# Performance work log

Measured on AMD Instinct MI355X. Metric: run time of the kernel, lower is better.

## Reference

```python
import jax, jax.numpy as jnp
import numpy as np

HEADS = 16
DIM_HEAD = 64


def shift(x):
    # Transformer-XL relative shift trick. x: [..., i, j] -> [..., i, j]
    *lead, i, j = x.shape
    x = jnp.concatenate([x, jnp.zeros((*lead, i, i), x.dtype)], axis=-1)
    l = i + j - 1
    x = x.reshape(*lead, -1)
    pad = (-x.shape[-1]) % l
    x = jnp.concatenate([x, jnp.zeros((*lead, pad), x.dtype)], axis=-1)
    x = x.reshape(*lead, -1, l)
    return x[..., :i, i - 1:]


def setup_inputs() -> dict:
    key = jax.random.key(0)
    ks = jax.random.split(key, 6)
    b, t, d = 4, 1024, 1024
    mem_len = 1024
    s = 0.02
    return {
        "x": jax.random.normal(ks[0], (b, t, d), jnp.float32),
        "mem": jax.random.normal(ks[1], (b, mem_len, d), jnp.float32),
        "wq": jax.random.normal(ks[2], (d, d), jnp.float32) * s,
        "wkv": jax.random.normal(ks[3], (d, 2 * d), jnp.float32) * s,
        "wo": jax.random.normal(ks[4], (d, d), jnp.float32) * s,
        "bo": jnp.zeros((d,), jnp.float32),
        "rel_w": jax.random.normal(ks[5], (t + mem_len, HEADS, DIM_HEAD), jnp.float32) * s,
    }


def reference(x, mem, wq, wkv, wo, bo, rel_w):
    b, t, d = x.shape
    h, dh = HEADS, DIM_HEAD
    mem_len = mem.shape[1]
    scale = dh ** -0.5

    q = x @ wq                                  # [b,t,d]
    kv_in = jnp.concatenate([mem, x], axis=1)   # [b,t+mem,d]
    k, v = jnp.split(kv_in @ wkv, 2, axis=-1)

    to_heads = lambda z: z.reshape(b, -1, h, dh).transpose(0, 2, 1, 3)
    q, k, v = to_heads(q), to_heads(k), to_heads(v)  # [b,h,*,dh]

    dots = jnp.einsum('bhid,bhjd->bhij', q, k) * scale      # [b,h,t,t+mem]
    w = rel_w[: t + mem_len]                                 # [t+mem,h,dh]
    pos = shift(jnp.einsum('bhid,jhd->bhij', q, w) * scale)  # [b,h,t,t+mem]
    dots = dots + pos

    jdim = t + mem_len
    mask = jnp.triu(jnp.ones((t, jdim), bool), k=1 + mem_len)
    dots = jnp.where(mask[None, None], -jnp.inf, dots)
    attn = jax.nn.softmax(dots, axis=-1)

    out = jnp.einsum('bhij,bhjd->bhid', attn, v)
    out = out.transpose(0, 2, 1, 3).reshape(b, t, d)
    out = out @ wo + bo

    mem_next = jnp.concatenate([mem, x], axis=1)[:, -mem_len:]  # t == seq_len branch
    return out, mem_next
```

## Files before the change

### kernel.cpp

```cpp
#include <hip/hip_runtime.h>
#include <cstddef>
#include <cstdint>

#define B_DIM 4
#define T_DIM 1024
#define D_DIM 1024
#define H_DIM 16
#define DH 64
#define JDIM 2048
#define MEMLEN 1024
#define RELPAD 2176

typedef float floatx4 __attribute__((ext_vector_type(4)));
typedef short short8 __attribute__((ext_vector_type(8)));

static __device__ __forceinline__ short f2bf(float f) {
    union { float f; uint32_t u; } v; v.f = f;
    uint32_t r = (v.u + 0x7FFFu + ((v.u >> 16) & 1u)) >> 16;
    return (short)r;
}

static __device__ __forceinline__ void gl_lds16(const short* g, short* l) {
    __builtin_amdgcn_global_load_lds(
        (const __attribute__((address_space(1))) void*)g,
        (__attribute__((address_space(3))) void*)l, 16, 0, 0);
}

template <int CTRL>
static __device__ __forceinline__ float dpp_fmax(float v) {
    int y = __builtin_amdgcn_update_dpp(0, __builtin_bit_cast(int, v),
                                        CTRL, 0xF, 0xF, true);
    return fmaxf(v, __builtin_bit_cast(float, y));
}
static __device__ __forceinline__ float row16_max(float v) {
    v = dpp_fmax<0xB1>(v);
    v = dpp_fmax<0x4E>(v);
    v = dpp_fmax<0x124>(v);
    v = dpp_fmax<0x128>(v);
    return v;
}

__global__ __launch_bounds__(256) void prep_xmem(const float* __restrict__ x,
                                                 const float* __restrict__ mem,
                                                 float* __restrict__ mem_next,
                                                 short* __restrict__ kvb) {
    const size_t gid = (size_t)blockIdx.x * 256 + threadIdx.x;
    if (gid < 1048576) {
        const size_t idx = gid * 4;
        float4 v = *(const float4*)(x + idx);
        *(float4*)(mem_next + idx) = v;
        const int b = (int)(idx >> 20);
        const size_t r = idx & 1048575;
        short4 o;
        o.x = f2bf(v.x); o.y = f2bf(v.y); o.z = f2bf(v.z); o.w = f2bf(v.w);
        *(short4*)(kvb + (size_t)b * 2097152 + 1048576 + r) = o;
    } else {
        const size_t idx = (gid - 1048576) * 4;
        float4 v = *(const float4*)(mem + idx);
        const int b = (int)(idx >> 20);
        const size_t r = idx & 1048575;
        short4 o;
        o.x = f2bf(v.x); o.y = f2bf(v.y); o.z = f2bf(v.z); o.w = f2bf(v.w);
        *(short4*)(kvb + (size_t)b * 2097152 + r) = o;
    }
}

__global__ __launch_bounds__(256) void transpose_w3(
    const float* __restrict__ wq, const float* __restrict__ wkv,
    const float* __restrict__ wo, short* __restrict__ wkvqT,
    short* __restrict__ woT) {
    const int z = blockIdx.z;
    const int N = (z == 1) ? 2048 : 1024;
    if (blockIdx.y * 32 >= N) return;
    const float* w = (z == 0) ? wq : (z == 1) ? wkv : wo;
    short* wT = (z == 0) ? (wkvqT + (size_t)2048 * 1024) : (z == 1) ? wkvqT : woT;
    __shared__ float tile[32][33];
    const int k0 = blockIdx.x * 32, n0 = blockIdx.y * 32;
    const int tx = threadIdx.x, ty = threadIdx.y;
    for (int r = ty; r < 32; r += 8)
        tile[r][tx] = w[(size_t)(k0 + r) * N + n0 + tx];
    __syncthreads();
    for (int r = ty; r < 32; r += 8)
        wT[(size_t)(n0 + r) * 1024 + k0 + tx] = f2bf(tile[tx][r]);
}

__global__ __launch_bounds__(256) void convert_rel(const float* __restrict__ rel,
                                                   short* __restrict__ relb) {
    const int h = blockIdx.y;
    const int jp = blockIdx.x * 16 + (threadIdx.x >> 4);
    const int c = (threadIdx.x & 15) << 2;
    float4 v = make_float4(0.f, 0.f, 0.f, 0.f);
    if (jp < JDIM) v = *(const float4*)(rel + ((size_t)jp * H_DIM + h) * DH + c);
    short4 o;
    o.x = f2bf(v.x); o.y = f2bf(v.y); o.z = f2bf(v.z); o.w = f2bf(v.w);
    *(short4*)(relb + ((size_t)h * RELPAD + jp) * DH + c) = o;
}

template <int CMODE>
__global__ __launch_bounds__(256) void mfma_gemm(
    const short* __restrict__ A, const short* __restrict__ Bt,
    const float* __restrict__ bias,
    short* __restrict__ C0, short* __restrict__ C1, short* __restrict__ C2,
    float* __restrict__ Cf) {
    constexpr int K = 1024;
    const int row0 = blockIdx.y << 7, col0 = blockIdx.x << 7;
    if (CMODE == 1 && col0 >= 2048 && (row0 & 2047) < 1024) return;

    __shared__ short ash[128 * 32];
    __shared__ short bsh[128 * 32];

    const int tid = threadIdx.x;
    const int w = tid >> 6, lane = tid & 63;
    const int l15 = lane & 15, quad = lane >> 4;
    const int wr = w >> 1, wc = w & 1;

    const int sk = (lane & 3) << 3;
    const short* ap0 = A + (size_t)(row0 + (w << 5) + (lane >> 2)) * K + sk;
    const short* ap1 = ap0 + (size_t)16 * K;
    const short* bp0 = Bt + (size_t)(col0 + (w << 5) + (lane >> 2)) * K + sk;
    const short* bp1 = bp0 + (size_t)16 * K;

    floatx4 acc[4][4] = {};

    for (int k0 = 0; k0 < K; k0 += 32) {
        __syncthreads();
        gl_lds16(ap0 + k0, ash + (w << 10));
        gl_lds16(ap1 + k0, ash + (w << 10) + 512);
        gl_lds16(bp0 + k0, bsh + (w << 10));
        gl_lds16(bp1 + k0, bsh + (w << 10) + 512);
        __syncthreads();

        short8 af[4];
#pragma unroll
        for (int mt = 0; mt < 4; ++mt)
            af[mt] = *(const short8*)&ash[(((wr << 6) + (mt << 4) + l15) << 5) + (quad << 3)];
#pragma unroll
        for (int nt = 0; nt < 4; ++nt) {
            short8 bf = *(const short8*)&bsh[(((wc << 6) + (nt << 4) + l15) << 5) + (quad << 3)];
#pragma unroll
            for (int mt = 0; mt < 4; ++mt)
                acc[mt][nt] = __builtin_amdgcn_mfma_f32_16x16x32_bf16(af[mt], bf, acc[mt][nt], 0, 0, 0);
        }
    }

#pragma unroll
    for (int nt = 0; nt < 4; ++nt) {
        const int col = col0 + (wc << 6) + (nt << 4) + l15;
        float bv = (CMODE == 2) ? bias[col] : 0.f;
#pragma unroll
        for (int mt = 0; mt < 4; ++mt) {
#pragma unroll
            for (int rr = 0; rr < 4; ++rr) {
                const int row = row0 + (wr << 6) + (mt << 4) + (quad << 2) + rr;
                const float val = acc[mt][nt][rr];
                if (CMODE == 1) {
                    int b = row >> 11, j = row & 2047;
                    if (col < 1024) {
                        int h = col >> 6, c = col & 63;
                        C0[(((size_t)b * H_DIM + h) * JDIM + j) * DH + c] = f2bf(val);
                    } else if (col < 2048) {
                        int n2 = col - 1024, h = n2 >> 6, c = n2 & 63;
                        C1[(((size_t)b * H_DIM + h) * DH + c) * JDIM + j] = f2bf(val);
                    } else {
                        int n2 = col - 2048, h = n2 >> 6, c = n2 & 63;
                        int i = j - 1024;
                        C2[(((size_t)b * H_DIM + h) * T_DIM + i) * DH + c] =
                            f2bf(val * 0.18033688f);
                    }
                } else {
                    Cf[(size_t)row * 1024 + col] = val + bv;
                }
            }
        }
    }
}

__global__ __launch_bounds__(256, 4) void flash_attn(
    const short* __restrict__ qb, const short* __restrict__ kb,
    const short* __restrict__ vTb, const short* __restrict__ relb,
    short* __restrict__ ob) {
    __shared__ short kshf[8 * 512];
    __shared__ short vshf[8 * 512];
    __shared__ short rshf[3 * 8 * 512];

    const int tid = threadIdx.x;
    const int w = tid >> 6;
    const int lane = tid & 63;
    const int l15 = lane & 15, quad = lane >> 4;
    const int bh = blockIdx.y, h = bh & 15, b = bh >> 4;
    const int xt = blockIdx.x;
    const int itile = ((xt >> 2) + ((xt & 3) << 2) + (((blockIdx.y >> 4) & 3) << 2)) & 15;
    const int i0 = itile << 6;
    const int goff = 3 - w;

    const short* kb_b = kb + (size_t)bh * JDIM * DH;
    const short* vT_b = vTb + (size_t)bh * DH * JDIM;
    const short* rel_b = relb + (size_t)h * RELPAD * DH;

    const short* qrow = qb + ((size_t)bh * T_DIM + i0 + (w << 4) + l15) * DH;
    const short8 a_q0 = *(const short8*)(qrow + (quad << 3));
    const short8 a_q1 = *(const short8*)(qrow + 32 + (quad << 3));

    const int kc0 = w, kc1 = w + 4;
    const short* kp0 = kb_b + (size_t)(((kc0 >> 1) << 4) + l15) * DH + (kc0 & 1) * 32 + (quad << 3);
    const short* kp1 = kb_b + (size_t)(((kc1 >> 1) << 4) + l15) * DH + (kc1 & 1) * 32 + (quad << 3);
    const short* vp0 = vT_b + (size_t)(((kc0 >> 1) << 4) + l15) * JDIM + (kc0 & 1) * 32 + (quad << 3);
    const short* vp1 = vT_b + (size_t)(((kc1 >> 1) << 4) + l15) * JDIM + (kc1 & 1) * 32 + (quad << 3);
    const int base00 = 960 - i0;

    gl_lds16(kp0, kshf + (kc0 << 9));
    gl_lds16(kp1, kshf + (kc1 << 9));
    gl_lds16(vp0, vshf + (kc0 << 9));
    gl_lds16(vp1, vshf + (kc1 << 9));
    kp0 += 64 * DH; kp1 += 64 * DH; vp0 += 64; vp1 += 64;
#pragma unroll
    for (int s = 0; s < 4; ++s) {
        const int c4 = w + (s << 2);
        const short* rp = rel_b + (size_t)(base00 + ((c4 >> 1) << 4) + l15) * DH +
                          (c4 & 1) * 32 + (quad << 3);
        gl_lds16(rp, rshf + (c4 << 9));
    }
    const short* rw0 = rel_b + (size_t)(base00 + 128 + ((w >> 1) << 4) + l15) * DH +
                       (w & 1) * 32 + (quad << 3);
    const short* rw1 = rel_b + (size_t)(base00 + 128 + (((w + 4) >> 1) << 4) + l15) * DH +
                       ((w + 4) & 1) * 32 + (quad << 3);
    __syncthreads();

    short8 ones8;
#pragma unroll
    for (int z = 0; z < 8; ++z) ones8[z] = (short)0x3F80;

    int srcl[4], gsel[4];
#pragma unroll
    for (int r = 0; r < 4; ++r) {
        const int t = l15 - (quad << 2) - r + 15;
        gsel[r] = t >> 4;
        srcl[r] = (quad << 4) | (t & 15);
    }

    floatx4 o_acc[4] = {};
    float m_r[4], l_r[4];
#pragma unroll
    for (int r = 0; r < 4; ++r) { m_r[r] = -3.0e38f; l_r[r] = 0.f; }

    const int jt_end = itile + 17;
    int s0 = 0, s1 = 1, s2 = 2;

    for (int jt = 0; jt < jt_end; ++jt) {
        floatx4 s_acc[4];
#pragma unroll
        for (int nt = 0; nt < 4; ++nt) {
            short8 bk0 = *(const short8*)&kshf[((nt << 1) << 9) + (lane << 3)];
            short8 bk1 = *(const short8*)&kshf[(((nt << 1) + 1) << 9) + (lane << 3)];
            floatx4 acc = {0.f, 0.f, 0.f, 0.f};
            acc = __builtin_amdgcn_mfma_f32_16x16x32_bf16(a_q0, bk0, acc, 0, 0, 0);
            acc = __builtin_amdgcn_mfma_f32_16x16x32_bf16(a_q1, bk1, acc, 0, 0, 0);
            s_acc[nt] = acc;
        }

        floatx4 G[5];
#pragma unroll
        for (int gi = 0; gi < 5; ++gi) {
            const int rb = gi + goff;
            const int seg = (rb & 4) ? s1 : s0;
            const int ch = (seg << 3) + ((rb & 3) << 1);
            short8 br0 = *(const short8*)&rshf[(ch << 9) + (lane << 3)];
            short8 br1 = *(const short8*)&rshf[((ch + 1) << 9) + (lane << 3)];
            floatx4 acc = {0.f, 0.f, 0.f, 0.f};
            acc = __builtin_amdgcn_mfma_f32_16x16x32_bf16(a_q0, br0, acc, 0, 0, 0);
            G[gi] = __builtin_amdgcn_mfma_f32_16x16x32_bf16(a_q1, br1, acc, 0, 0, 0);
        }

        uint32_t pk[4][4];
#pragma unroll
        for (int gi = 0; gi < 4; ++gi)
#pragma unroll
            for (int r = 0; r < 4; ++r) {
                uint32_t g0 = __builtin_bit_cast(uint32_t, G[gi][r]);
                uint32_t g1 = __builtin_bit_cast(uint32_t, G[gi + 1][r]);
                pk[gi][r] = (g0 & 0xFFFF0000u) | (g1 >> 16);
            }
#pragma unroll
        for (int nt = 0; nt < 4; ++nt)
#pragma unroll
            for (int r = 0; r < 4; ++r) {
                uint32_t pv = (uint32_t)__shfl((int)pk[nt][r], srcl[r], 64);
                uint32_t gb = gsel[r] ? (pv << 16) : (pv & 0xFFFF0000u);
                s_acc[nt][r] = s_acc[nt][r] + __builtin_bit_cast(float, gb);
            }
        if (jt == jt_end - 1) {
#pragma unroll
            for (int nt = 0; nt < 4; ++nt) {
                const int u = (nt << 4) + l15;
#pragma unroll
                for (int r = 0; r < 4; ++r) {
                    const int v = (w << 4) + (quad << 2) + r;
                    if (u > v) s_acc[nt][r] = -3.0e38f;
                }
            }
        }

        __syncthreads();
        if (jt + 1 < jt_end) {
            gl_lds16(kp0, kshf + (kc0 << 9));
            gl_lds16(kp1, kshf + (kc1 << 9));
            gl_lds16(rw0, rshf + (s2 << 12) + (w << 9));
            gl_lds16(rw1, rshf + (s2 << 12) + ((w + 4) << 9));
            kp0 += 64 * DH; kp1 += 64 * DH; rw0 += 64 * DH; rw1 += 64 * DH;
        }

        short* pshp = rshf + (s0 << 12);

        float tm[4];
        bool need = false;
#pragma unroll
        for (int r = 0; r < 4; ++r) {
            tm[r] = fmaxf(fmaxf(s_acc[0][r], s_acc[1][r]),
                          fmaxf(s_acc[2][r], s_acc[3][r]));
            need |= (tm[r] > m_r[r] + 8.0f);
        }
        if (__any((int)need)) {
#pragma unroll
            for (int r = 0; r < 4; ++r) {
                const float t = row16_max(tm[r]);
                const float mx = fmaxf(m_r[r], t);
                const float alpha = __builtin_amdgcn_exp2f(m_r[r] - mx);
                m_r[r] = mx;
                l_r[r] *= alpha;
#pragma unroll
                for (int ct = 0; ct < 4; ++ct) o_acc[ct][r] *= alpha;
            }
        }
#pragma unroll
        for (int r = 0; r < 4; ++r) {
            const int prow = (w << 4) + (quad << 2) + r;
            char* rowb = (char*)pshp + (prow << 7);
            const int swz = (prow & 7) << 4;
#pragma unroll
            for (int nt = 0; nt < 4; ++nt) {
                const float p = __builtin_amdgcn_exp2f(s_acc[nt][r] - m_r[r]);
                *(short*)(rowb + ((((nt << 5) + (l15 << 1))) ^ swz)) = f2bf(p);
            }
        }

        const int arow = (w << 4) + l15;
        const char* arowb = (const char*)pshp + (arow << 7);
        const int asw = (l15 & 7) << 4;
        const short8 a_p0 = *(const short8*)(arowb + ((quad << 4) ^ asw));
        const short8 a_p1 = *(const short8*)(arowb + ((64 + (quad << 4)) ^ asw));
        floatx4 ls = {0.f, 0.f, 0.f, 0.f};
        ls = __builtin_amdgcn_mfma_f32_16x16x32_bf16(a_p0, ones8, ls, 0, 0, 0);
        ls = __builtin_amdgcn_mfma_f32_16x16x32_bf16(a_p1, ones8, ls, 0, 0, 0);
#pragma unroll
        for (int r = 0; r < 4; ++r) l_r[r] += ls[r];
#pragma unroll
        for (int ct = 0; ct < 4; ++ct) {
            short8 bv0 = *(const short8*)&vshf[((ct << 1) << 9) + (lane << 3)];
            short8 bv1 = *(const short8*)&vshf[(((ct << 1) + 1) << 9) + (lane << 3)];
            o_acc[ct] = __builtin_amdgcn_mfma_f32_16x16x32_bf16(a_p0, bv0, o_acc[ct], 0, 0, 0);
            o_acc[ct] = __builtin_amdgcn_mfma_f32_16x16x32_bf16(a_p1, bv1, o_acc[ct], 0, 0, 0);
        }

        __syncthreads();
        if (jt + 1 < jt_end) {
            gl_lds16(vp0, vshf + (kc0 << 9));
            gl_lds16(vp1, vshf + (kc1 << 9));
            vp0 += 64; vp1 += 64;
        }
        const int t = s0; s0 = s1; s1 = s2; s2 = t;
    }

#pragma unroll
    for (int ct = 0; ct < 4; ++ct) {
#pragma unroll
        for (int r = 0; r < 4; ++r) {
            const int i = i0 + (w << 4) + (quad << 2) + r;
            const float val = o_acc[ct][r] / l_r[r];
            ob[((size_t)b * T_DIM + i) * D_DIM + h * DH + (ct << 4) + l15] = f2bf(val);
        }
    }
}

extern "C" void kernel_launch(void* const* d_in, const int* in_sizes, int n_in,
                              void* d_out, int out_size, void* d_ws, size_t ws_size,
                              hipStream_t stream) {
    const float* x = (const float*)d_in[0];
    const float* mem = (const float*)d_in[1];
    const float* wq = (const float*)d_in[2];
    const float* wkv = (const float*)d_in[3];
    const float* wo = (const float*)d_in[4];
    const float* bo = (const float*)d_in[5];
    const float* rel_w = (const float*)d_in[6];

    float* out = (float*)d_out;
    float* mem_next = out + (size_t)B_DIM * T_DIM * D_DIM;

    short* kvb = (short*)d_ws;
    short* qb = kvb + 8388608;
    short* kb = qb + 4194304;
    short* vTb = kb + 8388608;
    short* relb = vTb + 8388608;
    short* ob = relb + 2228224;
    short* wkvqT = ob + 4194304;
    short* woT = wkvqT + 3145728;

    hipLaunchKernelGGL(prep_xmem, dim3(8192), dim3(256), 0, stream,
                       x, mem, mem_next, kvb);

    hipLaunchKernelGGL(transpose_w3, dim3(32, 64, 3), dim3(32, 8), 0, stream,
                       wq, wkv, wo, wkvqT, woT);

    hipLaunchKernelGGL(convert_rel, dim3(RELPAD / 16, H_DIM), dim3(256), 0, stream,
                       rel_w, relb);

    hipLaunchKernelGGL((mfma_gemm<1>), dim3(24, 64), dim3(256), 0, stream,
                       kvb, wkvqT, nullptr, kb, vTb, qb, nullptr);

    hipLaunchKernelGGL(flash_attn, dim3(16, 64), dim3(256), 0, stream,
                       qb, kb, vTb, relb, ob);

    hipLaunchKernelGGL((mfma_gemm<2>), dim3(8, 32), dim3(256), 0, stream,
                       ob, woT, bo, nullptr, nullptr, nullptr, out);
}
```

Measured before the change: 312.9 us.

## Merge prep kernels into one launch, add setprio and byte-perm packing

Folds the three preprocessing kernels (x/mem conversion, weight transposes, rel-embedding conversion) into a single kernel dispatched by block index, so two launches and their gaps go away. In flash attention, MFMA sections are wrapped in s_setprio to favour waves issuing matrix work. The bf16 packing and select logic is replaced with v_perm byte permutes. The early return inside the merged kernel's transpose branch happens before a __syncthreads, but it is uniform per block so it stays safe.

```diff
diff --git a/kernel.cpp b/kernel.cpp
--- a/kernel.cpp
+++ b/kernel.cpp
@@ -40,60 +40,65 @@
     return v;
 }
 
-__global__ __launch_bounds__(256) void prep_xmem(const float* __restrict__ x,
-                                                 const float* __restrict__ mem,
-                                                 float* __restrict__ mem_next,
-                                                 short* __restrict__ kvb) {
-    const size_t gid = (size_t)blockIdx.x * 256 + threadIdx.x;
-    if (gid < 1048576) {
-        const size_t idx = gid * 4;
-        float4 v = *(const float4*)(x + idx);
-        *(float4*)(mem_next + idx) = v;
-        const int b = (int)(idx >> 20);
-        const size_t r = idx & 1048575;
+__global__ __launch_bounds__(256) void prep_all(
+    const float* __restrict__ x, const float* __restrict__ mem,
+    const float* __restrict__ rel,
+    float* __restrict__ mem_next, short* __restrict__ kvb,
+    const float* __restrict__ wq, const float* __restrict__ wkv,
+    const float* __restrict__ wo, short* __restrict__ wkvqT,
+    short* __restrict__ woT, short* __restrict__ relb) {
+    __shared__ float tile[32][33];
+    const int bx = blockIdx.x;
+    const int tid = threadIdx.x;
+
+    if (bx < 8192) {
+        const size_t gid = (size_t)bx * 256 + tid;
+        if (gid < 1048576) {
+            const size_t idx = gid * 4;
+            float4 v = *(const float4*)(x + idx);
+            *(float4*)(mem_next + idx) = v;
+            const int b = (int)(idx >> 20);
+            const size_t r = idx & 1048575;
+            short4 o;
+            o.x = f2bf(v.x); o.y = f2bf(v.y); o.z = f2bf(v.z); o.w = f2bf(v.w);
+            *(short4*)(kvb + (size_t)b * 2097152 + 1048576 + r) = o;
+        } else {
+            const size_t idx = (gid - 1048576) * 4;
+            float4 v = *(const float4*)(mem + idx);
+            const int b = (int)(idx >> 20);
+            const size_t r = idx & 1048575;
+            short4 o;
+            o.x = f2bf(v.x); o.y = f2bf(v.y); o.z = f2bf(v.z); o.w = f2bf(v.w);
+            *(short4*)(kvb + (size_t)b * 2097152 + r) = o;
+        }
+    } else if (bx < 14336) {
+        const int i = bx - 8192;
+        const int z = i >> 11;
+        const int rem = i & 2047;
+        const int gx = rem & 31, gy = rem >> 5;
+        const int N = (z == 1) ? 2048 : 1024;
+        if (gy * 32 >= N) return;
+        const float* w = (z == 0) ? wq : (z == 1) ? wkv : wo;
+        short* wT = (z == 0) ? (wkvqT + (size_t)2048 * 1024) : (z == 1) ? wkvqT : woT;
+        const int k0 = gx * 32, n0 = gy * 32;
+        const int tx = tid & 31, ty = tid >> 5;
+        for (int r = ty; r < 32; r += 8)
+            tile[r][tx] = w[(size_t)(k0 + r) * N + n0 + tx];
+        __syncthreads();
+        for (int r = ty; r < 32; r += 8)
+            wT[(size_t)(n0 + r) * 1024 + k0 + tx] = f2bf(tile[tx][r]);
+    } else {
+        const int i = bx - 14336;
+        const int gx = i % 136, gy = i / 136;
+        const int h = gy;
+        const int jp = gx * 16 + (tid >> 4);
+        const int c = (tid & 15) << 2;
+        float4 v = make_float4(0.f, 0.f, 0.f, 0.f);
+        if (jp < JDIM) v = *(const float4*)(rel + ((size_t)jp * H_DIM + h) * DH + c);
         short4 o;
         o.x = f2bf(v.x); o.y = f2bf(v.y); o.z = f2bf(v.z); o.w = f2bf(v.w);
-        *(short4*)(kvb + (size_t)b * 2097152 + 1048576 + r) = o;
-    } else {
-        const size_t idx = (gid - 1048576) * 4;
-        float4 v = *(const float4*)(mem + idx);
-        const int b = (int)(idx >> 20);
-        const size_t r = idx & 1048575;
-        short4 o;
-        o.x = f2bf(v.x); o.y = f2bf(v.y); o.z = f2bf(v.z); o.w = f2bf(v.w);
-        *(short4*)(kvb + (size_t)b * 2097152 + r) = o;
-    }
-}
-
-__global__ __launch_bounds__(256) void transpose_w3(
-    const float* __restrict__ wq, const float* __restrict__ wkv,
-    const float* __restrict__ wo, short* __restrict__ wkvqT,
-    short* __restrict__ woT) {
-    const int z = blockIdx.z;
-    const int N = (z == 1) ? 2048 : 1024;
-    if (blockIdx.y * 32 >= N) return;
-    const float* w = (z == 0) ? wq : (z == 1) ? wkv : wo;
-    short* wT = (z == 0) ? (wkvqT + (size_t)2048 * 1024) : (z == 1) ? wkvqT : woT;
-    __shared__ float tile[32][33];
-    const int k0 = blockIdx.x * 32, n0 = blockIdx.y * 32;
-    const int tx = threadIdx.x, ty = threadIdx.y;
-    for (int r = ty; r < 32; r += 8)
-        tile[r][tx] = w[(size_t)(k0 + r) * N + n0 + tx];
-    __syncthreads();
-    for (int r = ty; r < 32; r += 8)
-        wT[(size_t)(n0 + r) * 1024 + k0 + tx] = f2bf(tile[tx][r]);
-}
-
-__global__ __launch_bounds__(256) void convert_rel(const float* __restrict__ rel,
-                                                   short* __restrict__ relb) {
-    const int h = blockIdx.y;
-    const int jp = blockIdx.x * 16 + (threadIdx.x >> 4);
-    const int c = (threadIdx.x & 15) << 2;
-    float4 v = make_float4(0.f, 0.f, 0.f, 0.f);
-    if (jp < JDIM) v = *(const float4*)(rel + ((size_t)jp * H_DIM + h) * DH + c);
-    short4 o;
-    o.x = f2bf(v.x); o.y = f2bf(v.y); o.z = f2bf(v.z); o.w = f2bf(v.w);
-    *(short4*)(relb + ((size_t)h * RELPAD + jp) * DH + c) = o;
+        *(short4*)(relb + ((size_t)h * RELPAD + jp) * DH + c) = o;
+    }
 }
 
 template <int CMODE>
@@ -230,11 +235,12 @@
 #pragma unroll
     for (int z = 0; z < 8; ++z) ones8[z] = (short)0x3F80;
 
-    int srcl[4], gsel[4];
+    int srcl[4];
+    uint32_t psel[4];
 #pragma unroll
     for (int r = 0; r < 4; ++r) {
         const int t = l15 - (quad << 2) - r + 15;
-        gsel[r] = t >> 4;
+        psel[r] = (t >> 4) ? 0x01000404u : 0x03020404u;
         srcl[r] = (quad << 4) | (t & 15);
     }
 
@@ -247,6 +253,7 @@
     int s0 = 0, s1 = 1, s2 = 2;
 
     for (int jt = 0; jt < jt_end; ++jt) {
+        __builtin_amdgcn_s_setprio(1);
         floatx4 s_acc[4];
 #pragma unroll
         for (int nt = 0; nt < 4; ++nt) {
@@ -270,22 +277,22 @@
             acc = __builtin_amdgcn_mfma_f32_16x16x32_bf16(a_q0, br0, acc, 0, 0, 0);
             G[gi] = __builtin_amdgcn_mfma_f32_16x16x32_bf16(a_q1, br1, acc, 0, 0, 0);
         }
+        __builtin_amdgcn_s_setprio(0);
 
         uint32_t pk[4][4];
 #pragma unroll
         for (int gi = 0; gi < 4; ++gi)
 #pragma unroll
-            for (int r = 0; r < 4; ++r) {
-                uint32_t g0 = __builtin_bit_cast(uint32_t, G[gi][r]);
-                uint32_t g1 = __builtin_bit_cast(uint32_t, G[gi + 1][r]);
-                pk[gi][r] = (g0 & 0xFFFF0000u) | (g1 >> 16);
-            }
+            for (int r = 0; r < 4; ++r)
+                pk[gi][r] = __builtin_amdgcn_perm(
+                    __builtin_bit_cast(uint32_t, G[gi][r]),
+                    __builtin_bit_cast(uint32_t, G[gi + 1][r]), 0x07060302u);
 #pragma unroll
         for (int nt = 0; nt < 4; ++nt)
 #pragma unroll
             for (int r = 0; r < 4; ++r) {
                 uint32_t pv = (uint32_t)__shfl((int)pk[nt][r], srcl[r], 64);
-                uint32_t gb = gsel[r] ? (pv << 16) : (pv & 0xFFFF0000u);
+                uint32_t gb = __builtin_amdgcn_perm(0u, pv, psel[r]);
                 s_acc[nt][r] = s_acc[nt][r] + __builtin_bit_cast(float, gb);
             }
         if (jt == jt_end - 1) {
@@ -348,6 +355,7 @@
         const int asw = (l15 & 7) << 4;
         const short8 a_p0 = *(const short8*)(arowb + ((quad << 4) ^ asw));
         const short8 a_p1 = *(const short8*)(arowb + ((64 + (quad << 4)) ^ asw));
+        __builtin_amdgcn_s_setprio(1);
         floatx4 ls = {0.f, 0.f, 0.f, 0.f};
         ls = __builtin_amdgcn_mfma_f32_16x16x32_bf16(a_p0, ones8, ls, 0, 0, 0);
         ls = __builtin_amdgcn_mfma_f32_16x16x32_bf16(a_p1, ones8, ls, 0, 0, 0);
@@ -360,6 +368,7 @@
             o_acc[ct] = __builtin_amdgcn_mfma_f32_16x16x32_bf16(a_p0, bv0, o_acc[ct], 0, 0, 0);
             o_acc[ct] = __builtin_amdgcn_mfma_f32_16x16x32_bf16(a_p1, bv1, o_acc[ct], 0, 0, 0);
         }
+        __builtin_amdgcn_s_setprio(0);
 
         __syncthreads();
         if (jt + 1 < jt_end) {
@@ -404,14 +413,9 @@
     short* wkvqT = ob + 4194304;
     short* woT = wkvqT + 3145728;
 
-    hipLaunchKernelGGL(prep_xmem, dim3(8192), dim3(256), 0, stream,
-                       x, mem, mem_next, kvb);
-
-    hipLaunchKernelGGL(transpose_w3, dim3(32, 64, 3), dim3(32, 8), 0, stream,
-                       wq, wkv, wo, wkvqT, woT);
-
-    hipLaunchKernelGGL(convert_rel, dim3(RELPAD / 16, H_DIM), dim3(256), 0, stream,
-                       rel_w, relb);
+    hipLaunchKernelGGL(prep_all, dim3(16512), dim3(256), 0, stream,
+                       x, mem, rel_w, mem_next, kvb, wq, wkv, wo,
+                       wkvqT, woT, relb);
 
     hipLaunchKernelGGL((mfma_gemm<1>), dim3(24, 64), dim3(256), 0, stream,
                        kvb, wkvqT, nullptr, kb, vTb, qb, nullptr);
```

Result: no change. 315.0 us (+0.7%).
